# Kernel optimization log

Measured on AMD Instinct MI355X. Metric: run time of the kernel, lower is better.

The kernel has to match this reference:

```python
import jax, jax.numpy as jnp
import numpy as np

D = 1024   # rnn_size
H = 64     # pooling MLP hidden
B, C = 16, 1024


def setup_inputs() -> dict:
    key = jax.random.key(0)
    ks = jax.random.split(key, 12)
    s = 1.0 / np.sqrt(D)
    inp = {
        "encoder_outputs": jax.random.normal(ks[0], (B, C, D), jnp.float32),
        # Linear weights stored as [in, out] (y = x @ W + b), same math as torch Linear
        "Wf": jax.random.uniform(ks[1], (D, D), jnp.float32, -s, s),
        "bf": jax.random.uniform(ks[2], (D,), jnp.float32, -s, s),
        "Wg": jax.random.uniform(ks[3], (D, D), jnp.float32, -s, s),
        "bg": jax.random.uniform(ks[4], (D,), jnp.float32, -s, s),
        "Wx": jax.random.uniform(ks[5], (D, D), jnp.float32, -s, s),
        "bx": jax.random.uniform(ks[6], (D,), jnp.float32, -s, s),
        "W1": jax.random.uniform(ks[7], (D, H), jnp.float32, -s, s),
        "b1": jax.random.uniform(ks[8], (H,), jnp.float32, -s, s),
        "W2": jax.random.uniform(ks[9], (H, 1), jnp.float32, -1.0 / np.sqrt(H), 1.0 / np.sqrt(H)),
        "b2": jax.random.uniform(ks[10], (1,), jnp.float32, -1.0 / np.sqrt(H), 1.0 / np.sqrt(H)),
        # gamma is nn.Parameter(zeros(1)); use a nonzero value for a nontrivial baseline
        "gamma": jax.random.normal(ks[11], (1,), jnp.float32) * 0.1,
    }
    return inp


def reference(encoder_outputs, Wf, bf, Wg, bg, Wx, bx, W1, b1, W2, b2, gamma):
    x = encoder_outputs                                  # [B, C, D]
    q = jax.nn.relu(x @ Wf + bf)                         # proj_query [B, C, D]
    k = jax.nn.relu(x @ Wg + bg)                         # proj_key   [B, C, D]
    v = jax.nn.relu(x @ Wx + bx)                         # proj_value [B, C, D]
    energy = jnp.einsum('bid,bjd->bij', q, k)            # [B, C, C]
    attn = jax.nn.softmax(energy, axis=1)                # softmax over dim=1 (non-standard axis)
    # out = attention^T @ v : out[b,j,d] = sum_i attn[b,i,j] * v[b,i,d]
    out = jnp.einsum('bij,bid->bjd', attn, v)            # [B, C, D]
    out = gamma * out + x                                # gamma-residual
    # MLP attention pooling over C
    e2 = jax.nn.relu(x @ W1 + b1) @ W2 + b2              # [B, C, 1]
    w = jax.nn.softmax(e2[..., 0], axis=1)               # [B, C]
    return jnp.sum(out * w[..., None], axis=1)           # [B, D]
```

## Files before the change

### kernel.cpp

```cpp
#include <hip/hip_runtime.h>

#define B_ 16
#define C_ 1024
#define D_ 1024
#define H_ 64
#define M_ (B_*C_)

typedef __attribute__((ext_vector_type(8))) short bf16x8;
typedef __attribute__((ext_vector_type(8))) unsigned short ushortx8;
typedef __attribute__((ext_vector_type(4))) float f32x4;

__device__ __forceinline__ float wave_max(float v){
  #pragma unroll
  for (int o = 32; o > 0; o >>= 1) v = fmaxf(v, __shfl_xor(v, o));
  return v;
}
__device__ __forceinline__ float wave_sum(float v){
  #pragma unroll
  for (int o = 32; o > 0; o >>= 1) v += __shfl_xor(v, o);
  return v;
}

__device__ __forceinline__ ushort f2bf(float f){
  union { float f; unsigned u; } a; a.f = f;
  unsigned r = a.u + 0x7fff + ((a.u >> 16) & 1);
  return (ushort)(r >> 16);
}
__device__ __forceinline__ float bf2f(ushort h){
  union { unsigned u; float f; } a; a.u = ((unsigned)h) << 16; return a.f;
}

__device__ __forceinline__ void lds_cp16(const ushort* g, ushort* l){
  __builtin_amdgcn_global_load_lds(
      (const __attribute__((address_space(1))) void*)g,
      (__attribute__((address_space(3))) void*)l, 16, 0, 0);
}

__global__ __launch_bounds__(256) void prep_kernel(
    const float* __restrict__ x, const float* __restrict__ Wf,
    const float* __restrict__ Wg, const float* __restrict__ Wx,
    const float* __restrict__ W1,
    ushort* __restrict__ x_bf, ushort* __restrict__ wt,
    ushort* __restrict__ w1t)
{
  __shared__ float tile[32][33];
  const int blk = blockIdx.x;
  const int t = threadIdx.x;
  if (blk < 16384) {
    const int i = blk*256 + t;
    float4 v = ((const float4*)x)[i];
    ushort4 o;
    o.x = f2bf(v.x); o.y = f2bf(v.y); o.z = f2bf(v.z); o.w = f2bf(v.w);
    ((ushort4*)x_bf)[i] = o;
  } else if (blk < 16384 + 3072) {
    const int bb = blk - 16384;
    const int z = bb >> 10, rem = bb & 1023;
    const int n0 = (rem & 31)*32, k0 = (rem >> 5)*32;
    const float* W = (z == 0) ? Wf : (z == 1) ? Wg : Wx;
    ushort* Out = wt + (size_t)z*D_*D_;
    const int tx = t & 31, ty = t >> 5;
    #pragma unroll
    for (int i = 0; i < 32; i += 8)
      tile[ty+i][tx] = W[(size_t)(k0+ty+i)*D_ + n0+tx];
    __syncthreads();
    #pragma unroll
    for (int i = 0; i < 32; i += 8)
      Out[(size_t)(n0+ty+i)*D_ + k0+tx] = f2bf(tile[tx][ty+i]);
  } else {
    const int bb = blk - 16384 - 3072;
    const int n0 = (bb & 1)*32, k0 = (bb >> 1)*32;
    const int tx = t & 31, ty = t >> 5;
    #pragma unroll
    for (int i = 0; i < 32; i += 8)
      tile[ty+i][tx] = W1[(size_t)(k0+ty+i)*H_ + n0+tx];
    __syncthreads();
    #pragma unroll
    for (int i = 0; i < 32; i += 8)
      w1t[(size_t)(n0+ty+i)*D_ + k0+tx] = f2bf(tile[tx][ty+i]);
  }
}

__global__ __launch_bounds__(512, 2) void proj_kernel(
    const ushort* __restrict__ A, const ushort* __restrict__ Wt,
    const float* __restrict__ bf, const float* __restrict__ bg,
    const float* __restrict__ bx,
    ushort* __restrict__ q, ushort* __restrict__ k, ushort* __restrict__ v)
{
  __shared__ ushort As[4][8192];
  __shared__ ushort Bs[4][8192];
  const int t = threadIdx.x;
  const int lane = t & 63;
  const int wid  = t >> 6;
  const int wm = wid >> 2;
  const int wn = wid & 3;

  const int wg = blockIdx.x;
  const int sw = (wg & 7) * 96 + (wg >> 3);
  const int mI = sw / 12, nI = sw - mI*12;
  const int m0 = mI * 256, n0 = nI * 256;
  const int seg = n0 >> 10;
  const int nloc0 = n0 & 1023;

  const int srow = t >> 2;
  const int sfr  = (srow >> 1) & 3;
  const int schunk = ((t & 3) ^ sfr) * 8;
  const ushort* gA0 = A  + (size_t)(m0 + srow)*1024 + schunk;
  const ushort* gA1 = gA0 + (size_t)128*1024;
  const ushort* gB0 = Wt + (size_t)(n0 + srow)*1024 + schunk;
  const ushort* gB1 = gB0 + (size_t)128*1024;
  const int ldst = t * 8;

  const int quad = lane >> 4, l16 = lane & 15;
  const int fr4 = (l16 >> 1) & 3;
  const int aoff = (wm*128 + l16)*32 + ((quad ^ fr4) * 8);
  const int boff = (wn*64  + l16)*32 + ((quad ^ fr4) * 8);

  f32x4 acc[8][4] = {};

  #pragma unroll
  for (int tt = 0; tt < 3; ++tt) {
    const int ko = tt * 32;
    lds_cp16(gA0 + ko, &As[tt][ldst]);
    lds_cp16(gA1 + ko, &As[tt][4096 + ldst]);
    lds_cp16(gB0 + ko, &Bs[tt][ldst]);
    lds_cp16(gB1 + ko, &Bs[tt][4096 + ldst]);
  }
  asm volatile("s_waitcnt vmcnt(8)" ::: "memory");
  __builtin_amdgcn_s_barrier();

  for (int t0 = 0; t0 < 32; ++t0) {
    const int cur = t0 & 3;
    const ushort* Ab = As[cur];
    const ushort* Bb = Bs[cur];
    const int nxt = (t0 + 3) & 3;
    const int ko  = (t0 + 3) * 32;

    bf16x8 bfr[4], af[4];
    #pragma unroll
    for (int i = 0; i < 4; ++i) bfr[i] = *(const bf16x8*)&Bb[boff + i*512];
    #pragma unroll
    for (int i = 0; i < 4; ++i) af[i]  = *(const bf16x8*)&Ab[aoff + i*512];
    if (t0 < 29) {
      lds_cp16(gA0 + ko, &As[nxt][ldst]);
      lds_cp16(gA1 + ko, &As[nxt][4096 + ldst]);
    }
    __builtin_amdgcn_s_barrier();
    asm volatile("s_waitcnt lgkmcnt(0)" ::: "memory");
    __builtin_amdgcn_s_setprio(1);
    #pragma unroll
    for (int mt = 0; mt < 4; ++mt)
      #pragma unroll
      for (int nt = 0; nt < 4; ++nt)
        acc[mt][nt] = __builtin_amdgcn_mfma_f32_16x16x32_bf16(
            af[mt], bfr[nt], acc[mt][nt], 0, 0, 0);
    __builtin_amdgcn_s_setprio(0);
    __builtin_amdgcn_s_barrier();

    #pragma unroll
    for (int i = 0; i < 4; ++i) af[i] = *(const bf16x8*)&Ab[aoff + 2048 + i*512];
    if (t0 < 29) {
      lds_cp16(gB0 + ko, &Bs[nxt][ldst]);
      lds_cp16(gB1 + ko, &Bs[nxt][4096 + ldst]);
    }
    __builtin_amdgcn_s_barrier();
    asm volatile("s_waitcnt lgkmcnt(0)" ::: "memory");
    __builtin_amdgcn_s_setprio(1);
    #pragma unroll
    for (int mt = 0; mt < 4; ++mt)
      #pragma unroll
      for (int nt = 0; nt < 4; ++nt)
        acc[4+mt][nt] = __builtin_amdgcn_mfma_f32_16x16x32_bf16(
            af[mt], bfr[nt], acc[4+mt][nt], 0, 0, 0);
    __builtin_amdgcn_s_setprio(0);
    if (t0 < 29)       asm volatile("s_waitcnt vmcnt(8)" ::: "memory");
    else if (t0 == 29) asm volatile("s_waitcnt vmcnt(4)" ::: "memory");
    else if (t0 == 30) asm volatile("s_waitcnt vmcnt(0)" ::: "memory");
    __builtin_amdgcn_s_barrier();
  }

  const float* bp = (seg == 0) ? bf : (seg == 1) ? bg : bx;
  ushort* op      = (seg == 0) ? q  : (seg == 1) ? k  : v;
  const int gm_base = m0 + wm*128 + quad*4;
  const int gn_base = nloc0 + wn*64 + l16;
  float bv[4];
  #pragma unroll
  for (int nt = 0; nt < 4; ++nt) bv[nt] = bp[gn_base + nt*16];
  #pragma unroll
  for (int mt = 0; mt < 8; ++mt)
    #pragma unroll
    for (int rr = 0; rr < 4; ++rr) {
      const size_t rowoff = (size_t)(gm_base + mt*16 + rr) * 1024;
      #pragma unroll
      for (int nt = 0; nt < 4; ++nt)
        op[rowoff + gn_base + nt*16] =
            f2bf(fmaxf(acc[mt][nt][rr] + bv[nt], 0.f));
    }
}

__global__ __launch_bounds__(256, 4) void energy_kernel(
    const ushort* __restrict__ Km, const ushort* __restrict__ Qm,
    ushort* __restrict__ E)
{
  __shared__ ushort As[64*64];
  __shared__ ushort Bs[128*64];
  const int t = threadIdx.x;
  const int wid = t >> 6, lane = t & 63;
  const int m0 = blockIdx.y * 64, n0 = blockIdx.x * 128;
  const int bz = blockIdx.z;
  const ushort* Ab = Km + (size_t)bz * C_ * D_;
  const ushort* Bb = Qm + (size_t)bz * C_ * D_;

  const int srow = t >> 3;
  const int sch = ((t & 7) ^ (srow & 7)) * 8;
  const ushort* gaBase = Ab + (size_t)(m0 + srow)*1024 + sch;
  const ushort* gbBase = Bb + (size_t)(n0 + srow)*1024 + sch;

  const int quad = lane >> 4, l16 = lane & 15;
  const int cx0 = ((0*4 + quad) ^ (l16 & 7)) * 8;
  const int cx1 = ((1*4 + quad) ^ (l16 & 7)) * 8;
  const int brow0 = (wid*32 + l16)*64;

  f32x4 acc[4][2] = {};

  for (int k0 = 0; k0 < 1024; k0 += 64) {
    #pragma unroll
    for (int i = 0; i < 2; ++i)
      lds_cp16(gaBase + (size_t)(i*32)*1024, As + (8*wid + 32*i)*64);
    #pragma unroll
    for (int i = 0; i < 4; ++i)
      lds_cp16(gbBase + (size_t)(i*32)*1024, Bs + (8*wid + 32*i)*64);
    gaBase += 64; gbBase += 64;
    __syncthreads();
    #pragma unroll
    for (int h = 0; h < 2; ++h) {
      const int cx = h ? cx1 : cx0;
      bf16x8 af[4], bfr[2];
      #pragma unroll
      for (int i = 0; i < 4; ++i)
        af[i] = *(const bf16x8*)&As[(i*16 + l16)*64 + cx];
      #pragma unroll
      for (int i = 0; i < 2; ++i)
        bfr[i] = *(const bf16x8*)&Bs[brow0 + i*16*64 + cx];
      #pragma unroll
      for (int mt = 0; mt < 4; ++mt)
        #pragma unroll
        for (int nt = 0; nt < 2; ++nt)
          acc[mt][nt] = __builtin_amdgcn_mfma_f32_16x16x32_bf16(
              af[mt], bfr[nt], acc[mt][nt], 0, 0, 0);
    }
    __syncthreads();
  }

  ushort* O = E + (size_t)bz * C_ * C_;
  const int gm_base = m0 + quad*4;
  const int gn_base = n0 + wid*32 + l16;
  #pragma unroll
  for (int mt = 0; mt < 4; ++mt)
    #pragma unroll
    for (int rr = 0; rr < 4; ++rr) {
      const size_t rowoff = (size_t)(gm_base + mt*16 + rr) * 1024;
      #pragma unroll
      for (int nt = 0; nt < 2; ++nt)
        O[rowoff + gn_base + nt*16] = f2bf(acc[mt][nt][rr]);
    }
}

__device__ __forceinline__ int fsw(int row){
  return (row & 3) ^ ((row >> 2) & 3);
}
__global__ __launch_bounds__(256) void pool_mfma_kernel(
    const ushort* __restrict__ A, const ushort* __restrict__ Bt,
    const float* __restrict__ b1, const float* __restrict__ W2,
    float* __restrict__ e2out)
{
  __shared__ ushort As[128*32];
  __shared__ ushort Bs[64*32];
  const int t = threadIdx.x;
  const int wid = t >> 6, lane = t & 63;
  const int m0 = blockIdx.x * 128;

  const int r = t >> 2;
  const int kc = ((t & 3) ^ fsw(r)) * 8;
  const ushort* ga0 = A + (size_t)(m0 + r)*1024 + kc;
  const ushort* ga1 = ga0 + (size_t)64*1024;
  const ushort* gb0 = Bt + (size_t)r*1024 + kc;
  ushort* lA = As + wid*512;
  ushort* lB = Bs + wid*512;

  const int quad = lane >> 4, l16 = lane & 15;
  const int fr = fsw(l16);
  const int am0 = (wid*32 + l16)*32 + ((quad ^ fr)*8);
  const int bn0 = l16*32 + ((quad ^ fr)*8);

  f32x4 acc[2][4] = {};

  for (int k0 = 0; k0 < 1024; k0 += 32) {
    lds_cp16(ga0, lA); lds_cp16(ga1, lA + 2048);
    lds_cp16(gb0, lB);
    ga0 += 32; ga1 += 32; gb0 += 32;
    __syncthreads();
    bf16x8 af[2], bfr[4];
    #pragma unroll
    for (int i = 0; i < 2; ++i) af[i] = *(const bf16x8*)&As[am0 + i*512];
    #pragma unroll
    for (int i = 0; i < 4; ++i) bfr[i] = *(const bf16x8*)&Bs[bn0 + i*512];
    #pragma unroll
    for (int mt = 0; mt < 2; ++mt)
      #pragma unroll
      for (int nt = 0; nt < 4; ++nt)
        acc[mt][nt] = __builtin_amdgcn_mfma_f32_16x16x32_bf16(
            af[mt], bfr[nt], acc[mt][nt], 0, 0, 0);
    __syncthreads();
  }

  float b1v[4], w2v[4];
  #pragma unroll
  for (int nt = 0; nt < 4; ++nt) {
    b1v[nt] = b1[nt*16 + l16];
    w2v[nt] = W2[nt*16 + l16];
  }
  #pragma unroll
  for (int mt = 0; mt < 2; ++mt)
    #pragma unroll
    for (int rr = 0; rr < 4; ++rr) {
      float h = 0.f;
      #pragma unroll
      for (int nt = 0; nt < 4; ++nt)
        h += fmaxf(acc[mt][nt][rr] + b1v[nt], 0.f) * w2v[nt];
      #pragma unroll
      for (int o = 1; o < 16; o <<= 1) h += __shfl_xor(h, o);
      if (l16 == 0)
        e2out[m0 + wid*32 + mt*16 + quad*4 + rr] = h;
    }
}

__global__ __launch_bounds__(256) void fused_sm_kernel(
    const ushort* __restrict__ E, const float* __restrict__ w,
    float* __restrict__ u_part)
{
  __shared__ float ul[4][1024];
  const int b = blockIdx.y;
  const int strip = blockIdx.x;
  const int t = threadIdx.x, wv = t >> 6, lane = t & 63;
  const ushort* Eb = E + (size_t)b*C_*C_;
  const float* wb = w + (size_t)b*C_;
  float acc[2][8] = {};
  #pragma unroll
  for (int rj = 0; rj < 4; ++rj) {
    const int j = strip*16 + wv*4 + rj;
    const ushort* row = Eb + (size_t)j*C_;
    float vv[2][8];
    float m = -1e30f;
    #pragma unroll
    for (int c = 0; c < 2; ++c) {
      ushortx8 h = *(const ushortx8*)&row[c*512 + lane*8];
      #pragma unroll
      for (int kk = 0; kk < 8; ++kk) {
        vv[c][kk] = bf2f(h[kk]);
        m = fmaxf(m, vv[c][kk]);
      }
    }
    m = wave_max(m);
    float e[2][8];
    float s = 0.f;
    #pragma unroll
    for (int c = 0; c < 2; ++c)
      #pragma unroll
      for (int kk = 0; kk < 8; ++kk) {
        e[c][kk] = expf(vv[c][kk] - m);
        s += e[c][kk];
      }
    s = wave_sum(s);
    const float sc = wb[j] / s;
    #pragma unroll
    for (int c = 0; c < 2; ++c)
      #pragma unroll
      for (int kk = 0; kk < 8; ++kk) acc[c][kk] += sc * e[c][kk];
  }
  #pragma unroll
  for (int c = 0; c < 2; ++c)
    #pragma unroll
    for (int k4 = 0; k4 < 2; ++k4) {
      float4 o;
      o.x = acc[c][k4*4+0]; o.y = acc[c][k4*4+1];
      o.z = acc[c][k4*4+2]; o.w = acc[c][k4*4+3];
      *(float4*)&ul[wv][c*512 + lane*8 + k4*4] = o;
    }
  __syncthreads();
  float4 r0 = *(float4*)&ul[0][t*4];
  float4 r1 = *(float4*)&ul[1][t*4];
  float4 r2 = *(float4*)&ul[2][t*4];
  float4 r3 = *(float4*)&ul[3][t*4];
  float4 o;
  o.x = r0.x+r1.x+r2.x+r3.x; o.y = r0.y+r1.y+r2.y+r3.y;
  o.z = r0.z+r1.z+r2.z+r3.z; o.w = r0.w+r1.w+r2.w+r3.w;
  *(float4*)&u_part[((size_t)strip*B_ + b)*C_ + t*4] = o;
}

__global__ __launch_bounds__(256) void softmax_w_kernel(
    const float* __restrict__ e2in, float* __restrict__ w)
{
  __shared__ float redm[4];
  __shared__ float reds[4];
  const int b = blockIdx.x, t = threadIdx.x;
  const int lane = t & 63, wid = t >> 6;
  const float* row = e2in + (size_t)b*C_;
  float4 v = *(const float4*)&row[t*4];
  float m = fmaxf(fmaxf(v.x, v.y), fmaxf(v.z, v.w));
  m = wave_max(m);
  if (lane == 0) redm[wid] = m;
  __syncthreads();
  m = fmaxf(fmaxf(redm[0], redm[1]), fmaxf(redm[2], redm[3]));
  float e0 = expf(v.x - m), e1 = expf(v.y - m);
  float e2 = expf(v.z - m), e3 = expf(v.w - m);
  float s = e0 + e1 + e2 + e3;
  s = wave_sum(s);
  if (lane == 0) reds[wid] = s;
  __syncthreads();
  s = reds[0] + reds[1] + reds[2] + reds[3];
  const float inv = 1.0f / s;
  float4 o; o.x = e0*inv; o.y = e1*inv; o.z = e2*inv; o.w = e3*inv;
  *(float4*)&w[(size_t)b*C_ + t*4] = o;
}

__global__ __launch_bounds__(256) void final_part_kernel(
    const ushort* __restrict__ X, const ushort* __restrict__ V,
    const float* __restrict__ u_part, const float* __restrict__ w,
    const float* __restrict__ gamma, float* __restrict__ fpart)
{
  const int b = blockIdx.x, s = blockIdx.y;
  const int t = threadIdx.x;
  __shared__ float red[16][17];
  __shared__ float us[16];
  {
    const int ii = t & 15, g = t >> 4;
    float p = 0.f;
    #pragma unroll
    for (int q2 = 0; q2 < 4; ++q2) {
      const int sp = g*4 + q2;
      p += u_part[((size_t)sp*B_ + b)*C_ + s*16 + ii];
    }
    red[ii][g] = p;
  }
  __syncthreads();
  if (t < 16) {
    float s2 = 0.f;
    #pragma unroll
    for (int g = 0; g < 16; ++g) s2 += red[t][g];
    us[t] = s2;
  }
  __syncthreads();

  const int d0 = t * 4;
  const ushort* xb = X + (size_t)b*C_*D_;
  const ushort* vb = V + (size_t)b*C_*D_;
  const float* wb = w + (size_t)b*C_;
  float4 av = {0,0,0,0}, ax = {0,0,0,0};
  #pragma unroll
  for (int ii = 0; ii < 16; ++ii) {
    const int i = s*16 + ii;
    const float ui = us[ii], wi = wb[i];
    ushort4 vv = *(const ushort4*)&vb[(size_t)i*D_ + d0];
    ushort4 xv = *(const ushort4*)&xb[(size_t)i*D_ + d0];
    av.x += ui*bf2f(vv.x); av.y += ui*bf2f(vv.y);
    av.z += ui*bf2f(vv.z); av.w += ui*bf2f(vv.w);
    ax.x += wi*bf2f(xv.x); ax.y += wi*bf2f(xv.y);
    ax.z += wi*bf2f(xv.z); ax.w += wi*bf2f(xv.w);
  }
  const float g = gamma[0];
  float4 o;
  o.x = g*av.x + ax.x; o.y = g*av.y + ax.y;
  o.z = g*av.z + ax.z; o.w = g*av.w + ax.w;
  *(float4*)&fpart[((size_t)s*B_ + b)*D_ + d0] = o;
}

__global__ __launch_bounds__(256) void final_combine_kernel(
    const float* __restrict__ fpart, float* __restrict__ out)
{
  const int idx = blockIdx.x*256 + threadIdx.x;
  float s = 0.f;
  #pragma unroll 8
  for (int sp = 0; sp < 64; ++sp) s += fpart[(size_t)sp*B_*D_ + idx];
  out[idx] = s;
}

extern "C" void kernel_launch(void* const* d_in, const int* in_sizes, int n_in,
                              void* d_out, int out_size, void* d_ws, size_t ws_size,
                              hipStream_t stream) {
  (void)in_sizes; (void)n_in; (void)out_size; (void)ws_size;
  const float* x  = (const float*)d_in[0];
  const float* Wf = (const float*)d_in[1];
  const float* bf = (const float*)d_in[2];
  const float* Wg = (const float*)d_in[3];
  const float* bg = (const float*)d_in[4];
  const float* Wx = (const float*)d_in[5];
  const float* bx = (const float*)d_in[6];
  const float* W1 = (const float*)d_in[7];
  const float* b1 = (const float*)d_in[8];
  const float* W2 = (const float*)d_in[9];
  const float* gamma = (const float*)d_in[11];
  float* out = (float*)d_out;

  ushort* x_bf = (ushort*)d_ws;
  ushort* wt   = x_bf + (size_t)M_*D_;
  ushort* w1t  = wt + (size_t)3*D_*D_;
  ushort* q_bf = w1t + (size_t)H_*D_;
  ushort* k_bf = q_bf + (size_t)M_*D_;
  ushort* v_bf = k_bf + (size_t)M_*D_;
  ushort* E    = v_bf + (size_t)M_*D_;
  float*  e2b  = (float*)(E + (size_t)B_*C_*C_);
  float*  wbuf = e2b + M_;
  float*  u_part = wbuf + M_;
  float*  fpart  = (float*)E;

  prep_kernel<<<dim3(16384+3072+64), 256, 0, stream>>>(
      x, Wf, Wg, Wx, W1, x_bf, wt, w1t);

  proj_kernel<<<dim3(768), 512, 0, stream>>>(x_bf, wt, bf, bg, bx,
                                             q_bf, k_bf, v_bf);

  pool_mfma_kernel<<<dim3(M_/128), 256, 0, stream>>>(x_bf, w1t, b1, W2, e2b);
  softmax_w_kernel<<<dim3(B_), 256, 0, stream>>>(e2b, wbuf);

  energy_kernel<<<dim3(8,16,B_), 256, 0, stream>>>(k_bf, q_bf, E);
  fused_sm_kernel<<<dim3(64,B_), 256, 0, stream>>>(E, wbuf, u_part);

  final_part_kernel<<<dim3(B_,64), 256, 0, stream>>>(x_bf, v_bf, u_part, wbuf,
                                                     gamma, fpart);
  final_combine_kernel<<<dim3(M_/256), 256, 0, stream>>>(fpart, out);
}
```

Before: 331.9 us.

## Prefetch next-tile LDS fragments into registers and cut barriers in QKV GEMM loop

Restructures the QKV projection GEMM main loop so the B fragments and first-half A fragments for the next k-tile are read from LDS into registers during the current tile's second MFMA batch. The number of barriers per iteration drops from four to two, and the vmcnt waits are moved earlier. The aim is to hide LDS read latency behind MFMA work and cut synchronisation stalls. The cost is extra register pressure from double-buffered fragments, and the reworked wait counts add a risk of race conditions on buffer reuse.

Result: slower. 347.9 us (+4.8%).

```diff
diff --git a/kernel.cpp b/kernel.cpp
--- a/kernel.cpp
+++ b/kernel.cpp
@@ -126,56 +126,66 @@
     lds_cp16(gB1 + ko, &Bs[tt][4096 + ldst]);
   }
   asm volatile("s_waitcnt vmcnt(8)" ::: "memory");
-  __builtin_amdgcn_s_barrier();
+  asm volatile("s_barrier" ::: "memory");
+
+  bf16x8 cbf[4], ca0[4], nbf[4], na0[4];
+  #pragma unroll
+  for (int i = 0; i < 4; ++i) cbf[i] = *(const bf16x8*)&Bs[0][boff + i*512];
+  #pragma unroll
+  for (int i = 0; i < 4; ++i) ca0[i] = *(const bf16x8*)&As[0][aoff + i*512];
 
   for (int t0 = 0; t0 < 32; ++t0) {
-    const int cur = t0 & 3;
-    const ushort* Ab = As[cur];
-    const ushort* Bb = Bs[cur];
+    const ushort* Ab  = As[t0 & 3];
+    const ushort* AbN = As[(t0 + 1) & 3];
+    const ushort* BbN = Bs[(t0 + 1) & 3];
     const int nxt = (t0 + 3) & 3;
     const int ko  = (t0 + 3) * 32;
 
-    bf16x8 bfr[4], af[4];
-    #pragma unroll
-    for (int i = 0; i < 4; ++i) bfr[i] = *(const bf16x8*)&Bb[boff + i*512];
-    #pragma unroll
-    for (int i = 0; i < 4; ++i) af[i]  = *(const bf16x8*)&Ab[aoff + i*512];
     if (t0 < 29) {
       lds_cp16(gA0 + ko, &As[nxt][ldst]);
       lds_cp16(gA1 + ko, &As[nxt][4096 + ldst]);
     }
-    __builtin_amdgcn_s_barrier();
-    asm volatile("s_waitcnt lgkmcnt(0)" ::: "memory");
+    if (t0 < 29)       asm volatile("s_waitcnt vmcnt(6)" ::: "memory");
+    else if (t0 == 29) asm volatile("s_waitcnt vmcnt(4)" ::: "memory");
+    else if (t0 == 30) asm volatile("s_waitcnt vmcnt(0)" ::: "memory");
+    asm volatile("s_barrier" ::: "memory");
+
+    bf16x8 ca1[4];
+    #pragma unroll
+    for (int i = 0; i < 4; ++i) ca1[i] = *(const bf16x8*)&Ab[aoff + 2048 + i*512];
+    __builtin_amdgcn_sched_barrier(0);
     __builtin_amdgcn_s_setprio(1);
     #pragma unroll
     for (int mt = 0; mt < 4; ++mt)
       #pragma unroll
       for (int nt = 0; nt < 4; ++nt)
         acc[mt][nt] = __builtin_amdgcn_mfma_f32_16x16x32_bf16(
-            af[mt], bfr[nt], acc[mt][nt], 0, 0, 0);
+            ca0[mt], cbf[nt], acc[mt][nt], 0, 0, 0);
     __builtin_amdgcn_s_setprio(0);
-    __builtin_amdgcn_s_barrier();
-
-    #pragma unroll
-    for (int i = 0; i < 4; ++i) af[i] = *(const bf16x8*)&Ab[aoff + 2048 + i*512];
+
     if (t0 < 29) {
       lds_cp16(gB0 + ko, &Bs[nxt][ldst]);
       lds_cp16(gB1 + ko, &Bs[nxt][4096 + ldst]);
     }
-    __builtin_amdgcn_s_barrier();
-    asm volatile("s_waitcnt lgkmcnt(0)" ::: "memory");
+    if (t0 < 31) {
+      #pragma unroll
+      for (int i = 0; i < 4; ++i) nbf[i] = *(const bf16x8*)&BbN[boff + i*512];
+      #pragma unroll
+      for (int i = 0; i < 4; ++i) na0[i] = *(const bf16x8*)&AbN[aoff + i*512];
+    }
+    __builtin_amdgcn_sched_barrier(0);
     __builtin_amdgcn_s_setprio(1);
     #pragma unroll
     for (int mt = 0; mt < 4; ++mt)
       #pragma unroll
       for (int nt = 0; nt < 4; ++nt)
         acc[4+mt][nt] = __builtin_amdgcn_mfma_f32_16x16x32_bf16(
-            af[mt], bfr[nt], acc[4+mt][nt], 0, 0, 0);
+            ca1[mt], cbf[nt], acc[4+mt][nt], 0, 0, 0);
     __builtin_amdgcn_s_setprio(0);
-    if (t0 < 29)       asm volatile("s_waitcnt vmcnt(8)" ::: "memory");
-    else if (t0 == 29) asm volatile("s_waitcnt vmcnt(4)" ::: "memory");
-    else if (t0 == 30) asm volatile("s_waitcnt vmcnt(0)" ::: "memory");
-    __builtin_amdgcn_s_barrier();
+    asm volatile("s_barrier" ::: "memory");
+
+    #pragma unroll
+    for (int i = 0; i < 4; ++i) { cbf[i] = nbf[i]; ca0[i] = na0[i]; }
   }
 
   const float* bp = (seg == 0) ? bf : (seg == 1) ? bg : bx;
```
